# Kernel tuning notes

Measured on AMD Instinct MI355X. Metric: run time of the kernel, lower is better.

The kernel has to match this reference:

```python
import jax, jax.numpy as jnp
import numpy as np
import math

N_NODES = 2000
LOOKBACK = 24
IN_DIM = 16
EMB_DIM = 64
BATCH = 32
LN_EPS = 1e-5


def _layernorm(v, g, b):
    mu = jnp.mean(v, axis=-1, keepdims=True)
    var = jnp.var(v, axis=-1, keepdims=True)
    return (v - mu) * jax.lax.rsqrt(var + LN_EPS) * g + b


def setup_inputs() -> dict:
    key = jax.random.key(0)
    ks = jax.random.split(key, 12)
    td = LOOKBACK * IN_DIM  # 384
    s_in = 1.0 / math.sqrt(td)
    s_d = 1.0 / math.sqrt(IN_DIM)
    return {
        "x": jax.random.normal(ks[0], (BATCH, N_NODES, LOOKBACK, IN_DIM), jnp.float32),
        "Wq": jax.random.normal(ks[1], (td, EMB_DIM), jnp.float32) * s_in,
        "bq": jax.random.normal(ks[2], (EMB_DIM,), jnp.float32) * 0.01,
        "Wk": jax.random.normal(ks[3], (td, EMB_DIM), jnp.float32) * s_in,
        "bk": jax.random.normal(ks[4], (EMB_DIM,), jnp.float32) * 0.01,
        "g0": jnp.ones((EMB_DIM,), jnp.float32),
        "beta0": jnp.zeros((EMB_DIM,), jnp.float32),
        "g1": jnp.ones((EMB_DIM,), jnp.float32),
        "beta1": jnp.zeros((EMB_DIM,), jnp.float32),
        "normal": jax.random.normal(ks[5], (N_NODES, LOOKBACK, IN_DIM), jnp.float32),
        "Win": jax.random.normal(ks[6], (IN_DIM, IN_DIM), jnp.float32) * s_d,
    }


def reference(x, Wq, bq, Wk, bk, g0, beta0, g1, beta1, normal, Win):
    b, n, t, d = x.shape
    xf = x.reshape(b, n, t * d)
    # per-sample q/k linear + layernorm (batched over b)
    q1 = _layernorm(xf @ Wq + bq, g0, beta0)  # (b, n, e)
    k1 = _layernorm(xf @ Wk + bk, g1, beta1)  # (b, n, e)
    # node-mixing attention: softmax(q k^T / sqrt(num_nodes)) @ normal
    scores = jnp.einsum('bne,bme->bnm', q1, k1) / math.sqrt(n)
    A = jax.nn.softmax(scores, axis=-1)  # (b, n, n)
    data = jnp.einsum('bnm,mf->bnf', A, normal.reshape(n, t * d)).reshape(b, n, t, d)
    # RPPsAtt attention weights over time (general attention, output_len = 1)
    query = x[:, :, -1, :] @ Win  # (b, n, d)
    att = jnp.einsum('bnd,bntd->bnt', query, data)  # scores vs context
    weight = jax.nn.softmax(att, axis=-1)  # (b, n, t)
    # res = stack(weights).permute(0,1,3,2) -> (b, n, t, 1), broadcast-add
    return data + weight[..., None]
```

## Files before the change

kernel.cpp:

```cpp
#include <hip/hip_runtime.h>
#include <math.h>

#define B_   32
#define NN   2000
#define NP   2048
#define TT   24
#define TD   384
#define EE   64
#define SCALE 0.022360679774997896f

typedef __bf16 bf16;
typedef __bf16 bf16x8 __attribute__((ext_vector_type(8)));
typedef float  f32x4  __attribute__((ext_vector_type(4)));

typedef __attribute__((address_space(3))) unsigned int       lds_u32;
typedef const __attribute__((address_space(1))) unsigned int g_u32;

__device__ __forceinline__ void dma16(const void* g, void* l) {
    __builtin_amdgcn_global_load_lds((g_u32*)g, (lds_u32*)l, 16, 0, 0);
}

__device__ __forceinline__ bool input_is_bf16(const void* g0) {
    return *reinterpret_cast<const unsigned short*>(g0) == 0x3F80;
}

__device__ __forceinline__ float safexp(float v) {
    return __expf(fminf(fmaxf(v, -30.f), 30.f));
}

__device__ __forceinline__ bf16x8 ld_frag(const bf16* p) {
    return *reinterpret_cast<const bf16x8*>(p);
}

__device__ __forceinline__ bf16x8 cvt8_f32(const float* p) {
    f32x4 a = *reinterpret_cast<const f32x4*>(p);
    f32x4 b = *reinterpret_cast<const f32x4*>(p + 4);
    bf16x8 r;
    r[0]=(bf16)a[0]; r[1]=(bf16)a[1]; r[2]=(bf16)a[2]; r[3]=(bf16)a[3];
    r[4]=(bf16)b[0]; r[5]=(bf16)b[1]; r[6]=(bf16)b[2]; r[7]=(bf16)b[3];
    return r;
}

__global__ void pack_w_k(const void* Wqv, const void* Wkv, bf16* __restrict__ Wp,
                         const void* gflag) {
    bool bf = input_is_bf16(gflag);
    int o = blockIdx.x * 256 + threadIdx.x;
    if (o >= 12*8*64*8) return;
    int j  = o & 7;
    int l  = (o >> 3) & 63;
    int nt = (o >> 9) & 7;
    int ks = o >> 12;
    int k   = ks*32 + ((l >> 4) * 8) + j;
    int col = nt*16 + (l & 15);
    float v;
    if (bf) v = (col < 64) ? (float)((const bf16*)Wqv)[k*64 + col]
                           : (float)((const bf16*)Wkv)[k*64 + col - 64];
    else    v = (col < 64) ? ((const float*)Wqv)[k*64 + col]
                           : ((const float*)Wkv)[k*64 + col - 64];
    Wp[o] = (bf16)v;
}

__global__ void pack_v_k(const void* normalv, bf16* __restrict__ Vp, const void* gflag) {
    bool bf = input_is_bf16(gflag);
    int o = blockIdx.x * 256 + threadIdx.x;
    if (o >= 64*24*512) return;
    int j  = o & 7;
    int l  = (o >> 3) & 63;
    int nt = (o >> 9) % 24;
    int kb = o / (24*512);
    int key = kb*32 + ((l >> 4) * 8) + j;
    int col = nt*16 + (l & 15);
    float v = 0.f;
    if (key < NN)
        v = bf ? (float)((const bf16*)normalv)[key*TD + col]
               : ((const float*)normalv)[key*TD + col];
    Vp[o] = (bf16)v;
}

__global__ void calc_query_k(const void* xv, const void* Winv, float* __restrict__ Qry,
                             const void* gflag) {
    bool bf = input_is_bf16(gflag);
    int o = blockIdx.x * 256 + threadIdx.x;
    if (o >= B_*NP*16) return;
    int d2 = o & 15;
    int n  = (o >> 4) & (NP - 1);
    int b  = o >> 15;
    float acc = 0.f;
    if (n < NN) {
        size_t xoff = ((size_t)(b*NN + n))*TD + (TT-1)*16;
        if (bf) {
            const bf16* xr = (const bf16*)xv + xoff;
            const bf16* Wn = (const bf16*)Winv;
            #pragma unroll
            for (int d = 0; d < 16; ++d) acc += (float)xr[d] * (float)Wn[d*16 + d2];
        } else {
            const float* xr = (const float*)xv + xoff;
            const float* Wn = (const float*)Winv;
            #pragma unroll
            for (int d = 0; d < 16; ++d) acc += xr[d] * Wn[d*16 + d2];
        }
    }
    Qry[o] = acc;
}

__global__ __launch_bounds__(256) void proj_ln_k(
        const void* xv, const bf16* __restrict__ Wp,
        const void* bqv, const void* bkv,
        const void* g0v, const void* be0v,
        const void* g1v, const void* be1v,
        bf16* __restrict__ Qb, bf16* __restrict__ Kp) {
    __shared__ __align__(16) bf16 Wbuf[2][4096];
    bool bf = input_is_bf16(g0v);
    int mb = blockIdx.x, b = blockIdx.y;
    int w    = threadIdx.x >> 6;
    int lane = threadIdx.x & 63;
    int quad = lane >> 4, lq = lane & 15;

    int rowA = mb*64 + w*16 + lq;
    int xrow = rowA < NN ? rowA : NN - 1;

    bf16x8 afr[12];
    if (bf) {
        const bf16* xp = (const bf16*)xv + ((size_t)(b*NN + xrow))*TD + quad*8;
        #pragma unroll
        for (int ks = 0; ks < 12; ++ks) afr[ks] = ld_frag(xp + ks*32);
    } else {
        const float* xp = (const float*)xv + ((size_t)(b*NN + xrow))*TD + quad*8;
        #pragma unroll
        for (int ks = 0; ks < 12; ++ks) afr[ks] = cvt8_f32(xp + ks*32);
    }

    auto stage = [&](int ks, int bufi) {
        const char* g = (const char*)Wp + (size_t)ks*8192;
        for (int c = w; c < 8; c += 4)
            dma16(g + c*1024 + (size_t)lane*16, &Wbuf[bufi][c*512]);
    };
    stage(0, 0);

    f32x4 acc[8];
    #pragma unroll
    for (int nt = 0; nt < 8; ++nt) acc[nt] = (f32x4){0.f, 0.f, 0.f, 0.f};
    __syncthreads();

    for (int ks = 0; ks < 12; ++ks) {
        int cur = ks & 1;
        if (ks + 1 < 12) stage(ks + 1, cur ^ 1);
        const bf16* wb = Wbuf[cur];
        #pragma unroll
        for (int nt = 0; nt < 8; ++nt) {
            bf16x8 bfr = ld_frag(wb + nt*512 + lane*8);
            acc[nt] = __builtin_amdgcn_mfma_f32_16x16x32_bf16(afr[ks], bfr, acc[nt], 0, 0, 0);
        }
        __syncthreads();
    }

    #pragma unroll
    for (int nt = 0; nt < 8; ++nt) {
        int c = nt*16 + lq;
        float bias;
        if (bf) bias = (c < 64) ? (float)((const bf16*)bqv)[c] : (float)((const bf16*)bkv)[c-64];
        else    bias = (c < 64) ? ((const float*)bqv)[c] : ((const float*)bkv)[c-64];
        #pragma unroll
        for (int r = 0; r < 4; ++r) acc[nt][r] += bias;
    }
    float outn[8][4];
    #pragma unroll
    for (int g = 0; g < 2; ++g) {
        float s[4], sq[4];
        #pragma unroll
        for (int r = 0; r < 4; ++r) {
            float p = 0.f, p2 = 0.f;
            #pragma unroll
            for (int nt = 0; nt < 4; ++nt) {
                float v = acc[g*4 + nt][r];
                p += v; p2 += v*v;
            }
            s[r] = p; sq[r] = p2;
        }
        #pragma unroll
        for (int m = 1; m < 16; m <<= 1) {
            #pragma unroll
            for (int r = 0; r < 4; ++r) {
                s[r]  += __shfl_xor(s[r],  m, 16);
                sq[r] += __shfl_xor(sq[r], m, 16);
            }
        }
        #pragma unroll
        for (int r = 0; r < 4; ++r) {
            float mean = s[r] * (1.f/64.f);
            float var  = fmaxf(sq[r] * (1.f/64.f) - mean*mean, 0.f);
            float rs   = rsqrtf(var + 1e-5f);
            #pragma unroll
            for (int nt = 0; nt < 4; ++nt) {
                int c = nt*16 + lq;
                float gv, bv;
                if (g == 0) { gv = bf ? (float)((const bf16*)g0v)[c] : ((const float*)g0v)[c];
                              bv = bf ? (float)((const bf16*)be0v)[c] : ((const float*)be0v)[c]; }
                else        { gv = bf ? (float)((const bf16*)g1v)[c] : ((const float*)g1v)[c];
                              bv = bf ? (float)((const bf16*)be1v)[c] : ((const float*)be1v)[c]; }
                outn[g*4 + nt][r] = (acc[g*4 + nt][r] - mean) * rs * gv + bv;
            }
        }
    }
    int rowq = mb*64 + w*16 + quad*4;
    #pragma unroll
    for (int r = 0; r < 4; ++r) {
        int row = rowq + r;
        bool real = row < NN;
        size_t qbase = ((size_t)(b*NP + row))*EE;
        int kb2  = row >> 5;
        int half = (row >> 4) & 1;
        int lqk  = row & 15;
        #pragma unroll
        for (int nt = 0; nt < 4; ++nt) {
            Qb[qbase + nt*16 + lq] = (bf16)(real ? outn[nt][r] : 0.f);
            int col   = nt*16 + lq;
            int f     = half*2 + (col >> 5);
            int quadk = (col >> 3) & 3;
            size_t idx = (((size_t)(b*64 + kb2)*4 + f)*64 + quadk*16 + lqk)*8 + (col & 7);
            Kp[idx] = (bf16)(real ? outn[4 + nt][r] : 0.f);
        }
    }
}

__global__ __launch_bounds__(512, 4) void attn_k(
        const bf16* __restrict__ Qb, const bf16* __restrict__ Kp,
        const bf16* __restrict__ Vp, const float* __restrict__ Qry,
        void* outv, const void* gflag) {
    __shared__ __align__(16) char SM[41728];
    bf16*  PlB   = (bf16*)(SM);
    bf16*  scr   = (bf16*)(SM + 8192);
    float* eBuf  = (float*)(SM + 34304);
    float* denP  = (float*)(SM + 40960);
    float* dnInv = (float*)(SM + 41472);

    bool bf = input_is_bf16(gflag);
    int mb = blockIdx.x, b = blockIdx.y;
    int w    = threadIdx.x >> 6;
    int lane = threadIdx.x & 63;
    int quad = lane >> 4, lq = lane & 15;
    int rowbase = mb*64;
    int rt = w >> 1;
    int h  = w & 1;

    const bf16* qp = Qb + ((size_t)(b*NP + rowbase + rt*16 + lq))*EE + quad*8;
    bf16x8 aq0 = ld_frag(qp);
    bf16x8 aq1 = ld_frag(qp + 32);

    f32x4 acc[4][3];
    #pragma unroll
    for (int i = 0; i < 4; ++i)
        #pragma unroll
        for (int ct = 0; ct < 3; ++ct) acc[i][ct] = (f32x4){0.f, 0.f, 0.f, 0.f};
    float den[4] = {0.f, 0.f, 0.f, 0.f};

    const bf16* kg = Kp + (size_t)(b*64)*2048 + h*1024 + lane*8;
    const bf16* vg = Vp + (size_t)(w*3)*512 + lane*8;

    const int pb = (h*2 + (lq >> 3))*128 + quad*32 + (lq & 7);

    auto barrier_p = [&]() {
        asm volatile("s_waitcnt lgkmcnt(0)" ::: "memory");
        __builtin_amdgcn_s_barrier();
        __builtin_amdgcn_sched_barrier(0);
    };
    auto qk = [&](bf16x8 k0, bf16x8 k1) -> f32x4 {
        f32x4 s = (f32x4){0.f,0.f,0.f,0.f};
        s = __builtin_amdgcn_mfma_f32_16x16x32_bf16(aq0, k0, s, 0, 0, 0);
        s = __builtin_amdgcn_mfma_f32_16x16x32_bf16(aq1, k1, s, 0, 0, 0);
        return s;
    };
    auto emit_p = [&](f32x4 s, int buf, bool maskpad) {
        bf16* pw = PlB + buf*2048 + rt*512;
        #pragma unroll
        for (int r = 0; r < 4; ++r) {
            float e = safexp(s[r] * SCALE);
            if (!maskpad || h == 0) den[r] += e;
            pw[pb + r*8] = (bf16)e;
        }
    };
    auto pv = [&](int buf, bf16x8 v0, bf16x8 v1, bf16x8 v2) {
        const bf16* pl = PlB + buf*2048;
        #pragma unroll
        for (int rt2 = 0; rt2 < 4; ++rt2) {
            bf16x8 ap = ld_frag(pl + rt2*512 + lane*8);
            acc[rt2][0] = __builtin_amdgcn_mfma_f32_16x16x32_bf16(ap, v0, acc[rt2][0], 0, 0, 0);
            acc[rt2][1] = __builtin_amdgcn_mfma_f32_16x16x32_bf16(ap, v1, acc[rt2][1], 0, 0, 0);
            acc[rt2][2] = __builtin_amdgcn_mfma_f32_16x16x32_bf16(ap, v2, acc[rt2][2], 0, 0, 0);
        }
    };

    bf16x8 kA0 = ld_frag(kg), kA1 = ld_frag(kg + 512); kg += 2048;
    bf16x8 kB0 = ld_frag(kg), kB1 = ld_frag(kg + 512); kg += 2048;
    bf16x8 vB0 = ld_frag(vg), vB1 = ld_frag(vg + 512), vB2 = ld_frag(vg + 1024);
    vg += 12288;
    emit_p(qk(kA0, kA1), 0, false);
    barrier_p();

    for (int it = 0; it < 30; ++it) {
        kA0 = ld_frag(kg); kA1 = ld_frag(kg + 512); kg += 2048;
        bf16x8 vA0 = ld_frag(vg), vA1 = ld_frag(vg + 512), vA2 = ld_frag(vg + 1024);
        vg += 12288;
        pv(0, vB0, vB1, vB2);
        emit_p(qk(kB0, kB1), 1, false);
        barrier_p();
        kB0 = ld_frag(kg); kB1 = ld_frag(kg + 512); kg += 2048;
        vB0 = ld_frag(vg); vB1 = ld_frag(vg + 512); vB2 = ld_frag(vg + 1024);
        vg += 12288;
        pv(1, vA0, vA1, vA2);
        emit_p(qk(kA0, kA1), 0, false);
        barrier_p();
    }

    {
        kA0 = ld_frag(kg); kA1 = ld_frag(kg + 512);
        bf16x8 vA0 = ld_frag(vg), vA1 = ld_frag(vg + 512), vA2 = ld_frag(vg + 1024);
        vg += 12288;
        pv(0, vB0, vB1, vB2);
        emit_p(qk(kB0, kB1), 1, false);
        barrier_p();
        vB0 = ld_frag(vg); vB1 = ld_frag(vg + 512); vB2 = ld_frag(vg + 1024);
        pv(1, vA0, vA1, vA2);
        emit_p(qk(kA0, kA1), 0, true);
        barrier_p();
    }
    pv(0, vB0, vB1, vB2);

    #pragma unroll
    for (int r = 0; r < 4; ++r) {
        float s = den[r];
        s += __shfl_xor(s, 1, 16); s += __shfl_xor(s, 2, 16);
        s += __shfl_xor(s, 4, 16); s += __shfl_xor(s, 8, 16);
        den[r] = s;
    }
    if (lq == 0) {
        #pragma unroll
        for (int r = 0; r < 4; ++r) denP[h*64 + rt*16 + quad*4 + r] = den[r];
    }
    __syncthreads();

    const float* qryb = Qry + ((size_t)(b*NP + rowbase))*16 + lq;
    #pragma unroll
    for (int rt2 = 0; rt2 < 4; ++rt2) {
        float inv[4], qd[4];
        #pragma unroll
        for (int r = 0; r < 4; ++r) {
            int row = rt2*16 + quad*4 + r;
            inv[r] = 1.f / fmaxf(denP[row] + denP[64 + row], 1e-30f);
            qd[r]  = qryb[(size_t)row*16];
        }
        #pragma unroll
        for (int ct = 0; ct < 3; ++ct) {
            #pragma unroll
            for (int r = 0; r < 4; ++r) {
                float v = acc[rt2][ct][r] * inv[r];
                acc[rt2][ct][r] = v;
                float a = v * qd[r];
                a += __shfl_xor(a, 1, 16); a += __shfl_xor(a, 2, 16);
                a += __shfl_xor(a, 4, 16); a += __shfl_xor(a, 8, 16);
                float e = safexp(a);
                if (lq == 0) eBuf[(rt2*16 + quad*4 + r)*26 + (w*3 + ct)] = e;
            }
        }
    }
    __syncthreads();

    if (lane < 8) {
        int row = w*8 + lane;
        float s = 0.f;
        #pragma unroll
        for (int t = 0; t < 24; ++t) s += eBuf[row*26 + t];
        dnInv[row] = 1.f / fmaxf(s, 1e-30f);
    }
    __syncthreads();

    if (bf) {
        #pragma unroll
        for (int half = 0; half < 2; ++half) {
            #pragma unroll
            for (int rti = 0; rti < 2; ++rti) {
                int rt2 = half*2 + rti;
                #pragma unroll
                for (int ct = 0; ct < 3; ++ct) {
                    int t = w*3 + ct;
                    #pragma unroll
                    for (int r = 0; r < 4; ++r) {
                        int row = rt2*16 + quad*4 + r;
                        float wv = eBuf[row*26 + t] * dnInv[row];
                        scr[(size_t)(row - half*32)*408 + t*16 + lq] =
                            (bf16)(acc[rt2][ct][r] + wv);
                    }
                }
            }
            __syncthreads();
            bf16* og = (bf16*)outv + ((size_t)b*NN + rowbase + half*32)*TD;
            #pragma unroll
            for (int i = 0; i < 4; ++i) {
                int lrow = w*4 + i;
                int grow = rowbase + half*32 + lrow;
                if (grow < NN && lane < 48)
                    *reinterpret_cast<bf16x8*>(og + (size_t)lrow*TD + lane*8) =
                        *reinterpret_cast<const bf16x8*>(scr + (size_t)lrow*408 + lane*8);
            }
            __syncthreads();
        }
    } else {
        #pragma unroll
        for (int rt2 = 0; rt2 < 4; ++rt2) {
            #pragma unroll
            for (int ct = 0; ct < 3; ++ct) {
                int t = w*3 + ct;
                #pragma unroll
                for (int r = 0; r < 4; ++r) {
                    int row  = rt2*16 + quad*4 + r;
                    int grow = rowbase + row;
                    if (grow < NN) {
                        float wv = eBuf[row*26 + t] * dnInv[row];
                        ((float*)outv)[((size_t)(b*NN + grow))*TD + t*16 + lq] =
                            acc[rt2][ct][r] + wv;
                    }
                }
            }
        }
    }
}

extern "C" void kernel_launch(void* const* d_in, const int* in_sizes, int n_in,
                              void* d_out, int out_size, void* d_ws, size_t ws_size,
                              hipStream_t stream) {
    const void* x      = d_in[0];
    const void* Wq     = d_in[1];
    const void* bq     = d_in[2];
    const void* Wk     = d_in[3];
    const void* bk     = d_in[4];
    const void* g0     = d_in[5];
    const void* be0    = d_in[6];
    const void* g1     = d_in[7];
    const void* be1    = d_in[8];
    const void* normal = d_in[9];
    const void* Win    = d_in[10];

    char* ws = (char*)d_ws;
    bf16*  Qb  = (bf16*)(ws);
    bf16*  Kp  = (bf16*)(ws + 8388608);
    bf16*  Vp  = (bf16*)(ws + 16777216);
    bf16*  Wp  = (bf16*)(ws + 16777216 + 1638400);
    float* Qry = (float*)(ws + 16777216 + 1638400 + 98304);

    pack_w_k<<<dim3(192), dim3(256), 0, stream>>>(Wq, Wk, Wp, g0);
    pack_v_k<<<dim3(3072), dim3(256), 0, stream>>>(normal, Vp, g0);
    calc_query_k<<<dim3(4096), dim3(256), 0, stream>>>(x, Win, Qry, g0);
    proj_ln_k<<<dim3(32, 32), dim3(256), 0, stream>>>(x, Wp, bq, bk, g0, be0, g1, be1, Qb, Kp);
    attn_k<<<dim3(32, 32), dim3(512), 0, stream>>>(Qb, Kp, Vp, Qry, d_out, g0);
}
```

Baseline: 352.2 us.

## Deepen attention pipeline with four P slots and merge prep kernels

Grows the shared-memory P buffer from two slots to four, so each loop step computes and emits two key blocks and runs the PV MFMAs for the previous two, with one barrier per step instead of two. K and V fragments are loaded further ahead. The exponent uses exp2 with the scale folded into one constant, and the PV MFMA section runs at raised wave priority. Separately, the three small preprocessing kernels (W pack, V pack, query projection) become one kernel launch. The extra LDS per block may reduce how many blocks fit on a compute unit, and the longer prefetch raises register pressure.

```diff
diff --git a/kernel.cpp b/kernel.cpp
--- a/kernel.cpp
+++ b/kernel.cpp
@@ -8,6 +8,8 @@
 #define TD   384
 #define EE   64
 #define SCALE 0.022360679774997896f
+#define S2E   0.032259642f
+#define CLP   43.28f
 
 typedef __bf16 bf16;
 typedef __bf16 bf16x8 __attribute__((ext_vector_type(8)));
@@ -41,66 +43,62 @@
     return r;
 }
 
-__global__ void pack_w_k(const void* Wqv, const void* Wkv, bf16* __restrict__ Wp,
-                         const void* gflag) {
-    bool bf = input_is_bf16(gflag);
-    int o = blockIdx.x * 256 + threadIdx.x;
-    if (o >= 12*8*64*8) return;
-    int j  = o & 7;
-    int l  = (o >> 3) & 63;
-    int nt = (o >> 9) & 7;
-    int ks = o >> 12;
-    int k   = ks*32 + ((l >> 4) * 8) + j;
-    int col = nt*16 + (l & 15);
-    float v;
-    if (bf) v = (col < 64) ? (float)((const bf16*)Wqv)[k*64 + col]
-                           : (float)((const bf16*)Wkv)[k*64 + col - 64];
-    else    v = (col < 64) ? ((const float*)Wqv)[k*64 + col]
-                           : ((const float*)Wkv)[k*64 + col - 64];
-    Wp[o] = (bf16)v;
-}
-
-__global__ void pack_v_k(const void* normalv, bf16* __restrict__ Vp, const void* gflag) {
-    bool bf = input_is_bf16(gflag);
-    int o = blockIdx.x * 256 + threadIdx.x;
-    if (o >= 64*24*512) return;
-    int j  = o & 7;
-    int l  = (o >> 3) & 63;
-    int nt = (o >> 9) % 24;
-    int kb = o / (24*512);
-    int key = kb*32 + ((l >> 4) * 8) + j;
-    int col = nt*16 + (l & 15);
-    float v = 0.f;
-    if (key < NN)
-        v = bf ? (float)((const bf16*)normalv)[key*TD + col]
-               : ((const float*)normalv)[key*TD + col];
-    Vp[o] = (bf16)v;
-}
-
-__global__ void calc_query_k(const void* xv, const void* Winv, float* __restrict__ Qry,
-                             const void* gflag) {
-    bool bf = input_is_bf16(gflag);
-    int o = blockIdx.x * 256 + threadIdx.x;
-    if (o >= B_*NP*16) return;
-    int d2 = o & 15;
-    int n  = (o >> 4) & (NP - 1);
-    int b  = o >> 15;
-    float acc = 0.f;
-    if (n < NN) {
-        size_t xoff = ((size_t)(b*NN + n))*TD + (TT-1)*16;
-        if (bf) {
-            const bf16* xr = (const bf16*)xv + xoff;
-            const bf16* Wn = (const bf16*)Winv;
-            #pragma unroll
-            for (int d = 0; d < 16; ++d) acc += (float)xr[d] * (float)Wn[d*16 + d2];
-        } else {
-            const float* xr = (const float*)xv + xoff;
-            const float* Wn = (const float*)Winv;
-            #pragma unroll
-            for (int d = 0; d < 16; ++d) acc += xr[d] * Wn[d*16 + d2];
-        }
-    }
-    Qry[o] = acc;
+__global__ __launch_bounds__(256) void prep_k(
+        const void* Wqv, const void* Wkv, bf16* __restrict__ Wp,
+        const void* normalv, bf16* __restrict__ Vp,
+        const void* xv, const void* Winv, float* __restrict__ Qry,
+        const void* gflag) {
+    bool bfl = input_is_bf16(gflag);
+    int bid = blockIdx.x;
+    if (bid < 192) {
+        int o = bid*256 + threadIdx.x;
+        int j  = o & 7;
+        int l  = (o >> 3) & 63;
+        int nt = (o >> 9) & 7;
+        int ks = o >> 12;
+        int k   = ks*32 + ((l >> 4) * 8) + j;
+        int col = nt*16 + (l & 15);
+        float v;
+        if (bfl) v = (col < 64) ? (float)((const bf16*)Wqv)[k*64 + col]
+                                : (float)((const bf16*)Wkv)[k*64 + col - 64];
+        else     v = (col < 64) ? ((const float*)Wqv)[k*64 + col]
+                                : ((const float*)Wkv)[k*64 + col - 64];
+        Wp[o] = (bf16)v;
+    } else if (bid < 3264) {
+        int o = (bid - 192)*256 + threadIdx.x;
+        int j  = o & 7;
+        int l  = (o >> 3) & 63;
+        int nt = (o >> 9) % 24;
+        int kb = o / (24*512);
+        int key = kb*32 + ((l >> 4) * 8) + j;
+        int col = nt*16 + (l & 15);
+        float v = 0.f;
+        if (key < NN)
+            v = bfl ? (float)((const bf16*)normalv)[key*TD + col]
+                    : ((const float*)normalv)[key*TD + col];
+        Vp[o] = (bf16)v;
+    } else {
+        int o = (bid - 3264)*256 + threadIdx.x;
+        int d2 = o & 15;
+        int n  = (o >> 4) & (NP - 1);
+        int b  = o >> 15;
+        float acc = 0.f;
+        if (n < NN) {
+            size_t xoff = ((size_t)(b*NN + n))*TD + (TT-1)*16;
+            if (bfl) {
+                const bf16* xr = (const bf16*)xv + xoff;
+                const bf16* Wn = (const bf16*)Winv;
+                #pragma unroll
+                for (int d = 0; d < 16; ++d) acc += (float)xr[d] * (float)Wn[d*16 + d2];
+            } else {
+                const float* xr = (const float*)xv + xoff;
+                const float* Wn = (const float*)Winv;
+                #pragma unroll
+                for (int d = 0; d < 16; ++d) acc += xr[d] * Wn[d*16 + d2];
+            }
+        }
+        Qry[o] = acc;
+    }
 }
 
 __global__ __launch_bounds__(256) void proj_ln_k(
@@ -227,12 +225,12 @@
         const bf16* __restrict__ Qb, const bf16* __restrict__ Kp,
         const bf16* __restrict__ Vp, const float* __restrict__ Qry,
         void* outv, const void* gflag) {
-    __shared__ __align__(16) char SM[41728];
+    __shared__ __align__(16) char SM[49920];
     bf16*  PlB   = (bf16*)(SM);
-    bf16*  scr   = (bf16*)(SM + 8192);
-    float* eBuf  = (float*)(SM + 34304);
-    float* denP  = (float*)(SM + 40960);
-    float* dnInv = (float*)(SM + 41472);
+    bf16*  scr   = (bf16*)(SM + 16384);
+    float* eBuf  = (float*)(SM + 42496);
+    float* denP  = (float*)(SM + 49152);
+    float* dnInv = (float*)(SM + 49664);
 
     bool bf = input_is_bf16(gflag);
     int mb = blockIdx.x, b = blockIdx.y;
@@ -254,8 +252,9 @@
         for (int ct = 0; ct < 3; ++ct) acc[i][ct] = (f32x4){0.f, 0.f, 0.f, 0.f};
     float den[4] = {0.f, 0.f, 0.f, 0.f};
 
-    const bf16* kg = Kp + (size_t)(b*64)*2048 + h*1024 + lane*8;
-    const bf16* vg = Vp + (size_t)(w*3)*512 + lane*8;
+    const bf16* kbase = Kp + (size_t)(b*64)*2048;
+    const int koff = h*1024 + lane*8;
+    const int voff = w*1536 + lane*8;
 
     const int pb = (h*2 + (lq >> 3))*128 + quad*32 + (lq & 7);
 
@@ -264,23 +263,32 @@
         __builtin_amdgcn_s_barrier();
         __builtin_amdgcn_sched_barrier(0);
     };
-    auto qk = [&](bf16x8 k0, bf16x8 k1) -> f32x4 {
+    auto ldK = [&](int kb, bf16x8& k0, bf16x8& k1) {
+        const bf16* p = kbase + kb*2048 + koff;
+        k0 = ld_frag(p);
+        k1 = ld_frag(p + 512);
+    };
+    auto ldV = [&](int kb, bf16x8& v0, bf16x8& v1, bf16x8& v2) {
+        const bf16* p = Vp + kb*12288 + voff;
+        v0 = ld_frag(p);
+        v1 = ld_frag(p + 512);
+        v2 = ld_frag(p + 1024);
+    };
+    auto qk_emit = [&](bf16x8 k0, bf16x8 k1, int slot, bool maskpad) {
         f32x4 s = (f32x4){0.f,0.f,0.f,0.f};
         s = __builtin_amdgcn_mfma_f32_16x16x32_bf16(aq0, k0, s, 0, 0, 0);
         s = __builtin_amdgcn_mfma_f32_16x16x32_bf16(aq1, k1, s, 0, 0, 0);
-        return s;
-    };
-    auto emit_p = [&](f32x4 s, int buf, bool maskpad) {
-        bf16* pw = PlB + buf*2048 + rt*512;
+        bf16* pw = PlB + slot*2048 + rt*512;
         #pragma unroll
         for (int r = 0; r < 4; ++r) {
-            float e = safexp(s[r] * SCALE);
+            float e = exp2f(fminf(fmaxf(s[r]*S2E, -CLP), CLP));
             if (!maskpad || h == 0) den[r] += e;
             pw[pb + r*8] = (bf16)e;
         }
     };
-    auto pv = [&](int buf, bf16x8 v0, bf16x8 v1, bf16x8 v2) {
-        const bf16* pl = PlB + buf*2048;
+    auto pv = [&](int slot, bf16x8 v0, bf16x8 v1, bf16x8 v2) {
+        const bf16* pl = PlB + slot*2048;
+        __builtin_amdgcn_s_setprio(1);
         #pragma unroll
         for (int rt2 = 0; rt2 < 4; ++rt2) {
             bf16x8 ap = ld_frag(pl + rt2*512 + lane*8);
@@ -288,43 +296,42 @@
             acc[rt2][1] = __builtin_amdgcn_mfma_f32_16x16x32_bf16(ap, v1, acc[rt2][1], 0, 0, 0);
             acc[rt2][2] = __builtin_amdgcn_mfma_f32_16x16x32_bf16(ap, v2, acc[rt2][2], 0, 0, 0);
         }
-    };
-
-    bf16x8 kA0 = ld_frag(kg), kA1 = ld_frag(kg + 512); kg += 2048;
-    bf16x8 kB0 = ld_frag(kg), kB1 = ld_frag(kg + 512); kg += 2048;
-    bf16x8 vB0 = ld_frag(vg), vB1 = ld_frag(vg + 512), vB2 = ld_frag(vg + 1024);
-    vg += 12288;
-    emit_p(qk(kA0, kA1), 0, false);
+        __builtin_amdgcn_s_setprio(0);
+    };
+
+    bf16x8 kA0, kA1, kB0, kB1;
+    bf16x8 vA0, vA1, vA2, vB0, vB1, vB2;
+
+    ldK(0, kA0, kA1);
+    ldK(1, kB0, kB1);
+    ldV(0, vA0, vA1, vA2);
+    ldV(1, vB0, vB1, vB2);
+    qk_emit(kA0, kA1, 0, false);
+    qk_emit(kB0, kB1, 1, false);
+    ldK(2, kA0, kA1);
+    ldK(3, kB0, kB1);
     barrier_p();
 
-    for (int it = 0; it < 30; ++it) {
-        kA0 = ld_frag(kg); kA1 = ld_frag(kg + 512); kg += 2048;
-        bf16x8 vA0 = ld_frag(vg), vA1 = ld_frag(vg + 512), vA2 = ld_frag(vg + 1024);
-        vg += 12288;
-        pv(0, vB0, vB1, vB2);
-        emit_p(qk(kB0, kB1), 1, false);
+    for (int t = 1; t <= 30; ++t) {
+        int E = 2*t;
+        int sE = E & 3, sO = (E+1) & 3, sEm2 = (E-2) & 3, sOm2 = (E-1) & 3;
+        pv(sEm2, vA0, vA1, vA2);
+        ldV(E, vA0, vA1, vA2);
+        qk_emit(kA0, kA1, sE, false);
+        ldK(E+2, kA0, kA1);
+        pv(sOm2, vB0, vB1, vB2);
+        ldV(E+1, vB0, vB1, vB2);
+        qk_emit(kB0, kB1, sO, false);
+        ldK(E+3, kB0, kB1);
         barrier_p();
-        kB0 = ld_frag(kg); kB1 = ld_frag(kg + 512); kg += 2048;
-        vB0 = ld_frag(vg); vB1 = ld_frag(vg + 512); vB2 = ld_frag(vg + 1024);
-        vg += 12288;
-        pv(1, vA0, vA1, vA2);
-        emit_p(qk(kA0, kA1), 0, false);
-        barrier_p();
-    }
-
-    {
-        kA0 = ld_frag(kg); kA1 = ld_frag(kg + 512);
-        bf16x8 vA0 = ld_frag(vg), vA1 = ld_frag(vg + 512), vA2 = ld_frag(vg + 1024);
-        vg += 12288;
-        pv(0, vB0, vB1, vB2);
-        emit_p(qk(kB0, kB1), 1, false);
-        barrier_p();
-        vB0 = ld_frag(vg); vB1 = ld_frag(vg + 512); vB2 = ld_frag(vg + 1024);
-        pv(1, vA0, vA1, vA2);
-        emit_p(qk(kA0, kA1), 0, true);
-        barrier_p();
-    }
-    pv(0, vB0, vB1, vB2);
+    }
+
+    pv(0, vA0, vA1, vA2);
+    ldV(62, vA0, vA1, vA2);
+    qk_emit(kA0, kA1, 2, true);
+    pv(1, vB0, vB1, vB2);
+    barrier_p();
+    pv(2, vA0, vA1, vA2);
 
     #pragma unroll
     for (int r = 0; r < 4; ++r) {
@@ -447,9 +454,7 @@
     bf16*  Wp  = (bf16*)(ws + 16777216 + 1638400);
     float* Qry = (float*)(ws + 16777216 + 1638400 + 98304);
 
-    pack_w_k<<<dim3(192), dim3(256), 0, stream>>>(Wq, Wk, Wp, g0);
-    pack_v_k<<<dim3(3072), dim3(256), 0, stream>>>(normal, Vp, g0);
-    calc_query_k<<<dim3(4096), dim3(256), 0, stream>>>(x, Win, Qry, g0);
+    prep_k<<<dim3(7360), dim3(256), 0, stream>>>(Wq, Wk, Wp, normal, Vp, x, Win, Qry, g0);
     proj_ln_k<<<dim3(32, 32), dim3(256), 0, stream>>>(x, Wp, bq, bk, g0, be0, g1, be1, Qb, Kp);
     attn_k<<<dim3(32, 32), dim3(512), 0, stream>>>(Qb, Kp, Vp, Qry, d_out, g0);
 }
```

Result: faster. 340.2 us (-3.4%).
